# Kernel optimization log

Measured on AMD Instinct MI355X. Metric: run time of the kernel, lower is better.

## Reference

```python
import jax, jax.numpy as jnp
import numpy as np

N, F, S, D = 8, 16, 196, 1024
H = 8
HD = D // H
L = 1 + F * S  # global feature token + f*s patch tokens


def _ln(x, g, b, eps=1e-5):
    m = x.mean(-1, keepdims=True)
    v = ((x - m) ** 2).mean(-1, keepdims=True)
    return (x - m) / jnp.sqrt(v + eps) * g + b


def _attn(q, k, v, hd):
    s = jnp.einsum('bqd,bkd->bqk', q, k) / jnp.sqrt(jnp.asarray(hd, q.dtype))
    return jnp.einsum('bqk,bkd->bqd', jax.nn.softmax(s, axis=-1), v)


def setup_inputs() -> dict:
    key = jax.random.key(0)
    ks = jax.random.split(key, 8)
    sc = 0.02
    return {
        'x': jax.random.normal(ks[0], (N, L, D), jnp.float32),
        'W_in': jax.random.normal(ks[1], (D, D), jnp.float32) * sc,
        'b_in': jnp.zeros((D,), jnp.float32),
        'g_in': jnp.ones((D,), jnp.float32),
        'beta_in': jnp.zeros((D,), jnp.float32),
        'W_q': jax.random.normal(ks[2], (D, D), jnp.float32) * sc,
        'W_k': jax.random.normal(ks[3], (D, D), jnp.float32) * sc,
        'W_v': jax.random.normal(ks[4], (D, D), jnp.float32) * sc,
        'g_out': jnp.ones((D,), jnp.float32),
        'beta_out': jnp.zeros((D,), jnp.float32),
        'W_out': jax.random.normal(ks[5], (D, D), jnp.float32) * sc,
        'b_out': jnp.zeros((D,), jnp.float32),
        'att_type': 1,  # 1 == 'time', 0 == 'space' (static)
    }


def reference(x, W_in, b_in, g_in, beta_in, W_q, W_k, W_v, g_out, beta_out, W_out, b_out, att_type):
    n = x.shape[0]
    nh = n * H
    # in_fc: Linear + LayerNorm
    x = _ln(x @ W_in + b_in, g_in, beta_in)
    q, k, v = x @ W_q, x @ W_k, x @ W_v

    def split_heads(y):  # [n, L, D] -> [n*h, L, hd]
        return y.reshape(n, L, H, HD).transpose(0, 2, 1, 3).reshape(nh, L, HD)

    q, k, v = map(split_heads, (q, k, v))
    feat_q, q = q[:, :1], q[:, 1:]
    feat_k, k = k[:, :1], k[:, 1:]
    feat_v, v = v[:, :1], v[:, 1:]

    # token_att is computed in the original but never used (dead code):
    # token_att = _attn(feat_q, k, v, HD)

    if att_type == 1:  # time attention: windows of length F per spatial site
        qt = q.reshape(nh, F, S, HD).transpose(0, 2, 1, 3).reshape(nh * S, F, HD)
        kt = k.reshape(nh, F, S, HD).transpose(0, 2, 1, 3).reshape(nh * S, F, HD)
        vt = v.reshape(nh, F, S, HD).transpose(0, 2, 1, 3).reshape(nh * S, F, HD)
        fk = jnp.tile(feat_k, (S, 1, 1))  # torch .repeat(s,1,1)
        fv = jnp.tile(feat_v, (S, 1, 1))
        kk = jnp.concatenate((fk, kt), axis=1)  # [nh*s, 1+f, hd]
        vv = jnp.concatenate((fv, vt), axis=1)
        seq = _attn(qt, kk, vv, HD)  # [nh*s, f, hd]
        seq = seq.reshape(nh, S, F, HD).transpose(0, 2, 1, 3).reshape(nh, F * S, HD)
    else:  # space attention: windows of length S per frame
        qs = q.reshape(nh * F, S, HD)
        ks_ = k.reshape(nh * F, S, HD)
        vs = v.reshape(nh * F, S, HD)
        fk = jnp.tile(feat_k, (F, 1, 1))
        fv = jnp.tile(feat_v, (F, 1, 1))
        kk = jnp.concatenate((fk, ks_), axis=1)  # [nh*f, 1+s, hd]
        vv = jnp.concatenate((fv, vs), axis=1)
        seq = _attn(qs, kk, vv, HD)  # [nh*f, s, hd]
        seq = seq.reshape(nh, F * S, HD)

    out = jnp.concatenate((feat_q, seq), axis=1)  # [nh, L, hd]
    out = out.reshape(n, H, L, HD).transpose(0, 2, 1, 3).reshape(n, L, D)
    out = _ln(out, g_out, beta_out) @ W_out + b_out
    return out
```

## Files before the change

kernel.cpp:

```cpp
#include <hip/hip_runtime.h>
#include <stdint.h>

#define N_B 8
#define F_T 16
#define S_T 196
#define D_M 1024
#define H_N 8
#define HD  128
#define L_T 3137
#define M_R (N_B * L_T)
#define M_P 25216

typedef __attribute__((ext_vector_type(8))) short bf16x8;
typedef __attribute__((ext_vector_type(4))) float f32x4;

__device__ __forceinline__ float b2f(unsigned int u) {
  union { unsigned int i; float f; } x; x.i = u << 16; return x.f;
}
__device__ __forceinline__ unsigned short f2b(float f) {
  union { float f; unsigned int i; } x; x.f = f;
  unsigned int r = x.i + 0x7fffu + ((x.i >> 16) & 1u);
  return (unsigned short)(r >> 16);
}

__global__ __launch_bounds__(256) void convert_pad(const float* __restrict__ x,
                                                   unsigned short* __restrict__ xb,
                                                   int nreal) {
  int i = (blockIdx.x * 256 + threadIdx.x) * 4;
  float4 v;
  if (i < nreal) v = *(const float4*)(x + i);
  else { v.x = 0.f; v.y = 0.f; v.z = 0.f; v.w = 0.f; }
  ushort4 o;
  o.x = f2b(v.x); o.y = f2b(v.y); o.z = f2b(v.z); o.w = f2b(v.w);
  *(ushort4*)(xb + i) = o;
}

struct WP { const float* s[5]; unsigned short* d[5]; };
__global__ __launch_bounds__(256) void transpose5(WP p) {
  __shared__ float t[32][33];
  const int w = blockIdx.z;
  const float* W = p.s[w];
  unsigned short* Wt = p.d[w];
  const int tx = threadIdx.x, ty = threadIdx.y;
  const int n0 = blockIdx.x * 32, k0 = blockIdx.y * 32;
#pragma unroll
  for (int i = 0; i < 4; i++)
    t[ty + i * 8][tx] = W[(size_t)(k0 + ty + i * 8) * D_M + n0 + tx];
  __syncthreads();
#pragma unroll
  for (int i = 0; i < 4; i++)
    Wt[(size_t)(n0 + ty + i * 8) * D_M + k0 + tx] = f2b(t[tx][ty + i * 8]);
}

__device__ __forceinline__ void async16(const unsigned short* g, unsigned short* l) {
  __builtin_amdgcn_global_load_lds((const __attribute__((address_space(1))) void*)g,
                                   (__attribute__((address_space(3))) void*)l, 16, 0, 0);
}

struct Outs { void* p[3]; };

#define MFMA_Q(AV, MLO)                                                        \
  __builtin_amdgcn_s_setprio(1);                                               \
  _Pragma("unroll") for (int m_ = 0; m_ < 4; ++m_)                             \
      _Pragma("unroll") for (int n_ = 0; n_ < 4; ++n_)                         \
          acc[(MLO) + m_][n_] = __builtin_amdgcn_mfma_f32_16x16x32_bf16(       \
              AV[(MLO) + m_], bv[n_], acc[(MLO) + m_][n_], 0, 0, 0);           \
  __builtin_amdgcn_s_setprio(0);

#define TILE_ONE(T, BUF, STGB, STGA, VMN)                                      \
  do {                                                                         \
    const unsigned short* Ab = sA + (BUF) * 16384 + aOff;                      \
    const unsigned short* Bb = sB + (BUF) * 16384 + bOff;                      \
    if (STGB) {                                                                \
      async16(gB + ((T) + 1) * 64,          sBst + (1 - (BUF)) * 16384);       \
      async16(gB + ((T) + 1) * 64 + 65536,  sBst + (1 - (BUF)) * 16384 + 4096);\
    }                                                                          \
    _Pragma("unroll") for (int m_ = 0; m_ < 4; ++m_)                           \
        av0[m_] = *(const bf16x8*)(Ab + m_ * 1024 + sl0);                      \
    _Pragma("unroll") for (int n_ = 0; n_ < 4; ++n_)                           \
        bv[n_] = *(const bf16x8*)(Bb + n_ * 1024 + sl0);                       \
    _Pragma("unroll") for (int m_ = 0; m_ < 4; ++m_)                           \
        av1[m_] = *(const bf16x8*)(Ab + m_ * 1024 + sl1);                      \
    MFMA_Q(av0, 0)                                                             \
    if (STGB) {                                                                \
      async16(gB + ((T) + 1) * 64 + 131072, sBst + (1 - (BUF)) * 16384 + 8192);\
      async16(gB + ((T) + 1) * 64 + 196608, sBst + (1 - (BUF)) * 16384 + 12288);\
    }                                                                          \
    _Pragma("unroll") for (int m_ = 0; m_ < 4; ++m_)                           \
        av0[4 + m_] = *(const bf16x8*)(Ab + (4 + m_) * 1024 + sl0);            \
    _Pragma("unroll") for (int m_ = 0; m_ < 4; ++m_)                           \
        av1[4 + m_] = *(const bf16x8*)(Ab + (4 + m_) * 1024 + sl1);            \
    MFMA_Q(av0, 4)                                                             \
    asm volatile("s_waitcnt lgkmcnt(0)" ::: "memory");                         \
    __builtin_amdgcn_s_barrier();                                              \
    asm volatile("" ::: "memory");                                             \
    if (STGA) {                                                                \
      async16(gA + ((T) + 2) * 64,          sAst + (BUF) * 16384);             \
      async16(gA + ((T) + 2) * 64 + 65536,  sAst + (BUF) * 16384 + 4096);      \
    }                                                                          \
    _Pragma("unroll") for (int n_ = 0; n_ < 4; ++n_)                           \
        bv[n_] = *(const bf16x8*)(Bb + n_ * 1024 + sl1);                       \
    MFMA_Q(av1, 0)                                                             \
    if (STGA) {                                                                \
      async16(gA + ((T) + 2) * 64 + 131072, sAst + (BUF) * 16384 + 8192);      \
      async16(gA + ((T) + 2) * 64 + 196608, sAst + (BUF) * 16384 + 12288);     \
    }                                                                          \
    MFMA_Q(av1, 4)                                                             \
    if ((VMN) == 4)                                                            \
      asm volatile("s_waitcnt vmcnt(4) lgkmcnt(0)" ::: "memory");              \
    else if ((VMN) == 0)                                                       \
      asm volatile("s_waitcnt vmcnt(0) lgkmcnt(0)" ::: "memory");              \
    else                                                                       \
      asm volatile("s_waitcnt lgkmcnt(0)" ::: "memory");                       \
    __builtin_amdgcn_s_barrier();                                              \
    asm volatile("" ::: "memory");                                             \
  } while (0)

template <int MODE>
__global__ __launch_bounds__(512, 2) void gemm_bt(const unsigned short* __restrict__ A,
                                                  const unsigned short* __restrict__ Bt,
                                                  const float* __restrict__ bias,
                                                  Outs o, int Mreal) {
  __shared__ __align__(16) unsigned short lds[65536];
  unsigned short* sA = lds;
  unsigned short* sB = lds + 32768;

  const int tid = threadIdx.x;
  const int lane = tid & 63;
  const int wv = tid >> 6;
  const int wm = wv >> 2, wn = wv & 3;
  const int l15 = lane & 15, kg = lane >> 4;

  constexpr int NCT = (MODE == 3) ? 12 : 4;
  constexpr int NWG = 99 * NCT;
  constexpr int Q8 = NWG >> 3, R8 = NWG & 7;
  const int xcd = blockIdx.x & 7, off = blockIdx.x >> 3;
  const int lin = (xcd < R8 ? xcd * (Q8 + 1) : R8 * (Q8 + 1) + (xcd - R8) * Q8) + off;
  const int band = lin / 396;
  const int rem = lin - band * 396;
  const int rowBase = (rem >> 2) * 256;
  const int colBase = (band * 4 + (rem & 3)) * 256;

  const int srow = lane >> 3;
  const int gk = ((lane & 7) ^ srow) * 8;
  const unsigned short* gA = A + (size_t)(rowBase + wv * 8 + srow) * 1024 + gk;
  const unsigned short* gB = Bt + (size_t)(colBase + wv * 8 + srow) * 1024 + gk;
  unsigned short* sAst = sA + wv * 512 + lane * 8;
  unsigned short* sBst = sB + wv * 512 + lane * 8;

  const int aOff = (wm * 128 + l15) * 64;
  const int bOff = (wn * 64 + l15) * 64;
  const int sl0 = ((kg) ^ (l15 & 7)) * 8;
  const int sl1 = ((4 + kg) ^ (l15 & 7)) * 8;

  f32x4 acc[8][4] = {};
  bf16x8 av0[8], av1[8], bv[4];

#pragma unroll
  for (int i = 0; i < 4; i++) async16(gA + i * 65536, sAst + i * 4096);
#pragma unroll
  for (int i = 0; i < 4; i++) async16(gB + i * 65536, sBst + i * 4096);
#pragma unroll
  for (int i = 0; i < 4; i++) async16(gA + i * 65536 + 64, sAst + 16384 + i * 4096);
  asm volatile("s_waitcnt vmcnt(4)" ::: "memory");
  __builtin_amdgcn_s_barrier();
  asm volatile("" ::: "memory");

#pragma unroll 1
  for (int tp = 0; tp < 7; ++tp) {
    const int t0 = tp * 2;
    TILE_ONE(t0, 0, true, true, 4);
    TILE_ONE(t0 + 1, 1, true, true, 4);
  }
  TILE_ONE(14, 0, true, false, 0);
  TILE_ONE(15, 1, false, false, -1);

  __syncthreads();
  if (MODE == 2) {
    float* Cf = (float*)lds;
    float* outF = (float*)o.p[0];
#pragma unroll
    for (int p = 0; p < 2; ++p) {
      if (p) __syncthreads();
      if (wm == p) {
#pragma unroll
        for (int n = 0; n < 4; ++n) {
          const int col = wn * 64 + n * 16 + l15;
          const float bval = bias[colBase + col];
#pragma unroll
          for (int m = 0; m < 8; ++m)
#pragma unroll
            for (int r = 0; r < 4; ++r)
              Cf[(m * 16 + kg * 4 + r) * 256 + col] = acc[m][n][r] + bval;
        }
      }
      __syncthreads();
#pragma unroll
      for (int t2 = 0; t2 < 16; ++t2) {
        const int g = t2 * 512 + tid;
        const int row = g >> 6, ch = g & 63;
        const int grow = rowBase + p * 128 + row;
        if (grow < Mreal)
          *(float4*)(outF + (size_t)grow * 1024 + colBase + ch * 4) =
              *(const float4*)(Cf + row * 256 + ch * 4);
      }
    }
  } else {
    unsigned short* Cs = lds;
#pragma unroll
    for (int n = 0; n < 4; ++n) {
      const int col = wn * 64 + n * 16 + l15;
      const float bval = (MODE == 1) ? bias[colBase + col] : 0.f;
#pragma unroll
      for (int m = 0; m < 8; ++m)
#pragma unroll
        for (int r = 0; r < 4; ++r)
          Cs[(wm * 128 + m * 16 + kg * 4 + r) * 256 + col] = f2b(acc[m][n][r] + bval);
    }
    __syncthreads();
    unsigned short* C;
    int cbase;
    if (MODE == 3) { C = (unsigned short*)o.p[colBase >> 10]; cbase = colBase & 1023; }
    else { C = (unsigned short*)o.p[0]; cbase = colBase; }
#pragma unroll
    for (int t2 = 0; t2 < 16; ++t2) {
      const int g = t2 * 512 + tid;
      const int row = g >> 5, ch = g & 31;
      const int grow = rowBase + row;
      if (grow < Mreal)
        *(uint4*)(C + (size_t)grow * 1024 + cbase + ch * 8) =
            *(const uint4*)(Cs + row * 256 + ch * 8);
    }
  }
}

__global__ __launch_bounds__(256) void ln_kernel(const unsigned short* __restrict__ src,
                                                 const unsigned short* __restrict__ src0,
                                                 const float* __restrict__ g,
                                                 const float* __restrict__ beta,
                                                 unsigned short* __restrict__ out, int Mreal) {
  const int row = blockIdx.x, tid = threadIdx.x;
  unsigned short* op = out + (size_t)row * 1024 + tid * 4;
  if (row >= Mreal) {
    ushort4 z; z.x = 0; z.y = 0; z.z = 0; z.w = 0;
    *(ushort4*)op = z;
    return;
  }
  const unsigned short* s = src;
  if (src0 != nullptr && (row % L_T) == 0) s = src0;
  const unsigned short* ip = s + (size_t)row * 1024 + tid * 4;
  uint2 raw = *(const uint2*)ip;
  float x0 = b2f(raw.x & 0xffffu), x1 = b2f(raw.x >> 16);
  float x2 = b2f(raw.y & 0xffffu), x3 = b2f(raw.y >> 16);
  float sum = x0 + x1 + x2 + x3;
  float sq = x0 * x0 + x1 * x1 + x2 * x2 + x3 * x3;
#pragma unroll
  for (int off = 32; off > 0; off >>= 1) {
    sum += __shfl_down(sum, off);
    sq += __shfl_down(sq, off);
  }
  __shared__ float red[8];
  if ((tid & 63) == 0) { red[tid >> 6] = sum; red[4 + (tid >> 6)] = sq; }
  __syncthreads();
  const float ts = red[0] + red[1] + red[2] + red[3];
  const float tq = red[4] + red[5] + red[6] + red[7];
  const float mean = ts * (1.f / 1024.f);
  const float var = tq * (1.f / 1024.f) - mean * mean;
  const float rstd = rsqrtf(var + 1e-5f);
  const float4 gv = *(const float4*)(g + tid * 4);
  const float4 bv = *(const float4*)(beta + tid * 4);
  ushort4 o;
  o.x = f2b((x0 - mean) * rstd * gv.x + bv.x);
  o.y = f2b((x1 - mean) * rstd * gv.y + bv.y);
  o.z = f2b((x2 - mean) * rstd * gv.z + bv.z);
  o.w = f2b((x3 - mean) * rstd * gv.w + bv.w);
  *(ushort4*)op = o;
}

#define ATT_T_BLOCKS (64 * 49)
__global__ __launch_bounds__(256) void attn_kernel(const unsigned short* __restrict__ q,
                                                   const unsigned short* __restrict__ k,
                                                   const unsigned short* __restrict__ v,
                                                   unsigned short* __restrict__ out,
                                                   const int* __restrict__ att_type) {
  __shared__ __align__(16) char smem[22528];
  const int tid = threadIdx.x;
  const int bid = blockIdx.x;
  const int at = att_type[0];

  if (at == 1) {
    if (bid >= ATT_T_BLOCKS) return;
    const int lane = tid & 63, wv = tid >> 6;
    const int l15 = lane & 15, kg = lane >> 4;
    const int hb = bid / 49, sb = bid - hb * 49;
    const int s = sb * 4 + wv;
    const int n = hb >> 3, h = hb & 7;
    const int fi = (hb * S_T + s) & 63;
    const size_t frow = (size_t)(fi >> 3) * L_T;
    const int fcol = (fi & 7) * HD;
    const int qbase = n * L_T + 1 + s;
    const int hcol = h * HD;

    unsigned short* Pl = (unsigned short*)(smem + wv * 5632);
    unsigned short* Vl = (unsigned short*)(smem + wv * 5632 + 1024);

    {
      const int dim0 = l15 * 8;
#pragma unroll
      for (int p = 0; p < 5; p++) {
        const int key = p * 4 + kg;
        if (key < 17) {
          const unsigned short* vp = (key == 0)
              ? (v + frow * 1024 + fcol + dim0)
              : (v + (size_t)(qbase + (key - 1) * S_T) * 1024 + hcol + dim0);
          uint4 r = *(const uint4*)vp;
          unsigned int* wp = (unsigned int*)Vl + key * 65 + l15 * 4;
          wp[0] = r.x; wp[1] = r.y; wp[2] = r.z; wp[3] = r.w;
        }
      }
    }

    bf16x8 aq[4], bk0[4], bk1[4];
    {
      const unsigned short* qp = q + (size_t)(qbase + l15 * S_T) * 1024 + hcol + kg * 8;
      const unsigned short* kp = (l15 == 0)
          ? (k + frow * 1024 + fcol + kg * 8)
          : (k + (size_t)(qbase + (l15 - 1) * S_T) * 1024 + hcol + kg * 8);
      const unsigned short* kp1 = k + (size_t)(qbase + 15 * S_T) * 1024 + hcol + kg * 8;
#pragma unroll
      for (int t = 0; t < 4; t++) {
        aq[t] = *(const bf16x8*)(qp + t * 32);
        bk0[t] = *(const bf16x8*)(kp + t * 32);
        if (l15 == 0) bk1[t] = *(const bf16x8*)(kp1 + t * 32);
        else {
          bf16x8 z = {};
          bk1[t] = z;
        }
      }
    }

    f32x4 c0 = {}, c1 = {};
#pragma unroll
    for (int t = 0; t < 4; t++) {
      c0 = __builtin_amdgcn_mfma_f32_16x16x32_bf16(aq[t], bk0[t], c0, 0, 0, 0);
      c1 = __builtin_amdgcn_mfma_f32_16x16x32_bf16(aq[t], bk1[t], c1, 0, 0, 0);
    }

    const float scl = 0.08838834764831845f;
#pragma unroll
    for (int r = 0; r < 4; r++) {
      float v0 = c0[r] * scl;
      float k16 = __shfl(c1[r] * scl, lane & 48);
      float mx = v0;
#pragma unroll
      for (int m = 1; m < 16; m <<= 1) mx = fmaxf(mx, __shfl_xor(mx, m));
      mx = fmaxf(mx, k16);
      float p = __expf(v0 - mx);
      float p16 = __expf(k16 - mx);
      float sum = p;
#pragma unroll
      for (int m = 1; m < 16; m <<= 1) sum += __shfl_xor(sum, m);
      sum += p16;
      const float inv = 1.f / sum;
      const int row = kg * 4 + r;
      Pl[row * 32 + l15] = f2b(p * inv);
      Pl[row * 32 + 16 + l15] = (l15 == 0) ? f2b(p16 * inv) : (unsigned short)0;
    }

    bf16x8 ap = *(const bf16x8*)(Pl + l15 * 32 + kg * 8);
#pragma unroll
    for (int nt = 0; nt < 8; nt++) {
      const int dim = nt * 16 + l15;
      bf16x8 bvv;
#pragma unroll
      for (int j = 0; j < 8; j++) {
        const int key = kg * 8 + j;
        const int kc = (key < 17) ? key : 0;
        unsigned short raw = Vl[kc * 130 + dim];
        bvv[j] = (key < 17) ? (short)raw : (short)0;
      }
      f32x4 z = {};
      f32x4 o = __builtin_amdgcn_mfma_f32_16x16x32_bf16(ap, bvv, z, 0, 0, 0);
#pragma unroll
      for (int r = 0; r < 4; r++) {
        const int qi = kg * 4 + r;
        out[(size_t)(qbase + qi * S_T) * 1024 + hcol + nt * 16 + l15] = f2b(o[r]);
      }
    }
    return;
  }

  float (*qs)[132] = (float (*)[132])smem;
  float (*sc)[212] = (float (*)[212])(smem + 8448);
  const int hb = bid / 208;
  const int rem = bid - hb * 208;
  const int f = rem / 13, qc = rem - f * 13;
  const int n = hb >> 3, h = hb & 7;
  const int fi = (hb * F_T + f) & 63;
  const size_t frow = (size_t)(fi >> 3) * L_T;
  const int fcol = (fi & 7) * HD;
  const int kbase = n * L_T + 1 + f * S_T;
  const int qbase = kbase + qc * 16;
  const int nk = S_T + 1;
  const int nqv = (qc == 12) ? 4 : 16;
  const int hcol = h * HD;

  {
    const int i = tid >> 4, db = (tid & 15) * 8;
    float* dst = &qs[i][db];
    if (i < nqv) {
      const unsigned short* qp = q + (size_t)(qbase + i) * 1024 + hcol + db;
      uint4 r = *(const uint4*)qp;
      dst[0] = b2f(r.x & 0xffffu); dst[1] = b2f(r.x >> 16);
      dst[2] = b2f(r.y & 0xffffu); dst[3] = b2f(r.y >> 16);
      dst[4] = b2f(r.z & 0xffffu); dst[5] = b2f(r.z >> 16);
      dst[6] = b2f(r.w & 0xffffu); dst[7] = b2f(r.w >> 16);
    } else {
#pragma unroll
      for (int u = 0; u < 8; u++) dst[u] = 0.f;
    }
  }
  __syncthreads();

  const int nslot = 16 * nk;
  for (int slot = tid; slot < nslot; slot += 256) {
    const int i = slot / nk, j = slot - i * nk;
    const unsigned short* kp = (j == 0)
        ? (k + frow * 1024 + fcol)
        : (k + (size_t)(kbase + (j - 1)) * 1024 + hcol);
    float acc = 0.f;
#pragma unroll 4
    for (int d = 0; d < 128; d += 8) {
      uint4 r = *(const uint4*)(kp + d);
      acc += qs[i][d + 0] * b2f(r.x & 0xffffu);
      acc += qs[i][d + 1] * b2f(r.x >> 16);
      acc += qs[i][d + 2] * b2f(r.y & 0xffffu);
      acc += qs[i][d + 3] * b2f(r.y >> 16);
      acc += qs[i][d + 4] * b2f(r.z & 0xffffu);
      acc += qs[i][d + 5] * b2f(r.z >> 16);
      acc += qs[i][d + 6] * b2f(r.w & 0xffffu);
      acc += qs[i][d + 7] * b2f(r.w >> 16);
    }
    sc[i][j] = acc * 0.08838834764831845f;
  }
  __syncthreads();

  if (tid < 16) {
    const int i = tid;
    float m = -1e30f;
    for (int j = 0; j < nk; j++) m = fmaxf(m, sc[i][j]);
    float ssum = 0.f;
    for (int j = 0; j < nk; j++) {
      float e = __expf(sc[i][j] - m);
      sc[i][j] = e;
      ssum += e;
    }
    const float inv = 1.f / ssum;
    for (int j = 0; j < nk; j++) sc[i][j] *= inv;
  }
  __syncthreads();

  {
    const int i = tid >> 4, db = (tid & 15) * 8;
    float o[8];
#pragma unroll
    for (int u = 0; u < 8; u++) o[u] = 0.f;
    for (int j = 0; j < nk; j++) {
      const unsigned short* vp = (j == 0)
          ? (v + frow * 1024 + fcol + db)
          : (v + (size_t)(kbase + (j - 1)) * 1024 + hcol + db);
      const float p = sc[i][j];
      uint4 r = *(const uint4*)vp;
      o[0] += p * b2f(r.x & 0xffffu); o[1] += p * b2f(r.x >> 16);
      o[2] += p * b2f(r.y & 0xffffu); o[3] += p * b2f(r.y >> 16);
      o[4] += p * b2f(r.z & 0xffffu); o[5] += p * b2f(r.z >> 16);
      o[6] += p * b2f(r.w & 0xffffu); o[7] += p * b2f(r.w >> 16);
    }
    if (i < nqv) {
      unsigned short* op = out + (size_t)(qbase + i) * 1024 + hcol + db;
      uint4 w;
      w.x = (unsigned)f2b(o[0]) | ((unsigned)f2b(o[1]) << 16);
      w.y = (unsigned)f2b(o[2]) | ((unsigned)f2b(o[3]) << 16);
      w.z = (unsigned)f2b(o[4]) | ((unsigned)f2b(o[5]) << 16);
      w.w = (unsigned)f2b(o[6]) | ((unsigned)f2b(o[7]) << 16);
      *(uint4*)op = w;
    }
  }
}

extern "C" void kernel_launch(void* const* d_in, const int* in_sizes, int n_in,
                              void* d_out, int out_size, void* d_ws, size_t ws_size,
                              hipStream_t stream) {
  const float* x        = (const float*)d_in[0];
  const float* W_in     = (const float*)d_in[1];
  const float* b_in     = (const float*)d_in[2];
  const float* g_in     = (const float*)d_in[3];
  const float* beta_in  = (const float*)d_in[4];
  const float* W_q      = (const float*)d_in[5];
  const float* W_k      = (const float*)d_in[6];
  const float* W_v      = (const float*)d_in[7];
  const float* g_out    = (const float*)d_in[8];
  const float* beta_out = (const float*)d_in[9];
  const float* W_out    = (const float*)d_in[10];
  const float* b_out    = (const float*)d_in[11];
  const int* att_type   = (const int*)d_in[12];
  float* out = (float*)d_out;

  char* ws = (char*)d_ws;
  const size_t MB = (size_t)M_P * 1024 * 2;
  unsigned short* xb = (unsigned short*)(ws + 0 * MB);
  unsigned short* t1 = (unsigned short*)(ws + 1 * MB);
  unsigned short* xh = (unsigned short*)(ws + 2 * MB);
  unsigned short* kb = (unsigned short*)(ws + 3 * MB);
  unsigned short* vb = (unsigned short*)(ws + 4 * MB);
  unsigned short* wt = (unsigned short*)(ws + 5 * MB);
  const size_t WSZ = (size_t)1024 * 1024;
  unsigned short* wt_in  = wt;
  unsigned short* wqkv   = wt + 1 * WSZ;
  unsigned short* wt_out = wt + 4 * WSZ;

  convert_pad<<<M_P, 256, 0, stream>>>(x, xb, M_R * 1024);

  WP wp;
  wp.s[0] = W_in; wp.s[1] = W_q; wp.s[2] = W_k; wp.s[3] = W_v; wp.s[4] = W_out;
  wp.d[0] = wt_in;
  wp.d[1] = wqkv;
  wp.d[2] = wqkv + 1 * WSZ;
  wp.d[3] = wqkv + 2 * WSZ;
  wp.d[4] = wt_out;
  transpose5<<<dim3(32, 32, 5), dim3(32, 8), 0, stream>>>(wp);

  Outs o1; o1.p[0] = t1; o1.p[1] = nullptr; o1.p[2] = nullptr;
  gemm_bt<1><<<396, 512, 0, stream>>>(xb, wt_in, b_in, o1, M_P);
  ln_kernel<<<M_P, 256, 0, stream>>>(t1, nullptr, g_in, beta_in, xh, M_R);

  Outs oq; oq.p[0] = t1; oq.p[1] = kb; oq.p[2] = vb;
  gemm_bt<3><<<1188, 512, 0, stream>>>(xh, wqkv, nullptr, oq, M_P);

  attn_kernel<<<13312, 256, 0, stream>>>(t1, kb, vb, xb, att_type);
  ln_kernel<<<M_P, 256, 0, stream>>>(xb, t1, g_out, beta_out, xh, M_R);

  Outs oo; oo.p[0] = out; oo.p[1] = nullptr; oo.p[2] = nullptr;
  gemm_bt<2><<<396, 512, 0, stream>>>(xh, wt_out, b_out, oo, M_R);
}
```

Before: 539.1 us.

## Interleave LDS reads with MFMA phases via extra barriers and swizzle epilogue staging

Restructures the GEMM inner tile into four phases separated by workgroup barriers and partial lgkmcnt waits, so waves take turns between LDS fragment loads and MFMA bursts (ping-pong style). It also trims the A-fragment register arrays from 8 to 4 entries using a third buffer, which lowers register pressure. Separately, the epilogue staging of the C tile in LDS now uses an XOR swizzle to reduce bank conflicts on both the write and read-back. The extra barriers add synchronisation cost per tile, and the partial waits rely on exact instruction counts being correct.

After: 567.3 us. 5.2% more time.

```diff
diff --git a/kernel.cpp b/kernel.cpp
--- a/kernel.cpp
+++ b/kernel.cpp
@@ -59,18 +59,19 @@
 
 struct Outs { void* p[3]; };
 
-#define MFMA_Q(AV, MLO)                                                        \
+#define MFMA16(AV, MLO)                                                        \
   __builtin_amdgcn_s_setprio(1);                                               \
   _Pragma("unroll") for (int m_ = 0; m_ < 4; ++m_)                             \
       _Pragma("unroll") for (int n_ = 0; n_ < 4; ++n_)                         \
           acc[(MLO) + m_][n_] = __builtin_amdgcn_mfma_f32_16x16x32_bf16(       \
-              AV[(MLO) + m_], bv[n_], acc[(MLO) + m_][n_], 0, 0, 0);           \
+              AV[m_], bv[n_], acc[(MLO) + m_][n_], 0, 0, 0);                   \
   __builtin_amdgcn_s_setprio(0);
 
-#define TILE_ONE(T, BUF, STGB, STGA, VMN)                                      \
+#define TILE_P(T, BUF, STGB, STGA, VMN)                                        \
   do {                                                                         \
     const unsigned short* Ab = sA + (BUF) * 16384 + aOff;                      \
     const unsigned short* Bb = sB + (BUF) * 16384 + bOff;                      \
+              \
     if (STGB) {                                                                \
       async16(gB + ((T) + 1) * 64,          sBst + (1 - (BUF)) * 16384);       \
       async16(gB + ((T) + 1) * 64 + 65536,  sBst + (1 - (BUF)) * 16384 + 4096);\
@@ -81,37 +82,45 @@
         bv[n_] = *(const bf16x8*)(Bb + n_ * 1024 + sl0);                       \
     _Pragma("unroll") for (int m_ = 0; m_ < 4; ++m_)                           \
         av1[m_] = *(const bf16x8*)(Ab + m_ * 1024 + sl1);                      \
-    MFMA_Q(av0, 0)                                                             \
+    __builtin_amdgcn_s_barrier();                                              \
+    asm volatile("s_waitcnt lgkmcnt(4)" ::: "memory");                         \
+    MFMA16(av0, 0)                                                             \
+    __builtin_amdgcn_s_barrier();                                              \
+                    \
     if (STGB) {                                                                \
       async16(gB + ((T) + 1) * 64 + 131072, sBst + (1 - (BUF)) * 16384 + 8192);\
       async16(gB + ((T) + 1) * 64 + 196608, sBst + (1 - (BUF)) * 16384 + 12288);\
     }                                                                          \
     _Pragma("unroll") for (int m_ = 0; m_ < 4; ++m_)                           \
-        av0[4 + m_] = *(const bf16x8*)(Ab + (4 + m_) * 1024 + sl0);            \
+        av0[m_] = *(const bf16x8*)(Ab + (4 + m_) * 1024 + sl0);                \
     _Pragma("unroll") for (int m_ = 0; m_ < 4; ++m_)                           \
-        av1[4 + m_] = *(const bf16x8*)(Ab + (4 + m_) * 1024 + sl1);            \
-    MFMA_Q(av0, 4)                                                             \
+        av2[m_] = *(const bf16x8*)(Ab + (4 + m_) * 1024 + sl1);                \
+    __builtin_amdgcn_s_barrier();                                              \
     asm volatile("s_waitcnt lgkmcnt(0)" ::: "memory");                         \
-    __builtin_amdgcn_s_barrier();                                              \
-    asm volatile("" ::: "memory");                                             \
+    MFMA16(av0, 4)                                                             \
+    __builtin_amdgcn_s_barrier();                                              \
+                        \
     if (STGA) {                                                                \
       async16(gA + ((T) + 2) * 64,          sAst + (BUF) * 16384);             \
       async16(gA + ((T) + 2) * 64 + 65536,  sAst + (BUF) * 16384 + 4096);      \
     }                                                                          \
     _Pragma("unroll") for (int n_ = 0; n_ < 4; ++n_)                           \
         bv[n_] = *(const bf16x8*)(Bb + n_ * 1024 + sl1);                       \
-    MFMA_Q(av1, 0)                                                             \
+    __builtin_amdgcn_s_barrier();                                              \
+    asm volatile("s_waitcnt lgkmcnt(0)" ::: "memory");                         \
+    MFMA16(av1, 0)                                                             \
+    __builtin_amdgcn_s_barrier();                                              \
+                    \
     if (STGA) {                                                                \
       async16(gA + ((T) + 2) * 64 + 131072, sAst + (BUF) * 16384 + 8192);      \
       async16(gA + ((T) + 2) * 64 + 196608, sAst + (BUF) * 16384 + 12288);     \
     }                                                                          \
-    MFMA_Q(av1, 4)                                                             \
+    __builtin_amdgcn_s_barrier();                                              \
+    MFMA16(av2, 4)                                                             \
     if ((VMN) == 4)                                                            \
-      asm volatile("s_waitcnt vmcnt(4) lgkmcnt(0)" ::: "memory");              \
+      asm volatile("s_waitcnt vmcnt(4)" ::: "memory");                         \
     else if ((VMN) == 0)                                                       \
-      asm volatile("s_waitcnt vmcnt(0) lgkmcnt(0)" ::: "memory");              \
-    else                                                                       \
-      asm volatile("s_waitcnt lgkmcnt(0)" ::: "memory");                       \
+      asm volatile("s_waitcnt vmcnt(0)" ::: "memory");                         \
     __builtin_amdgcn_s_barrier();                                              \
     asm volatile("" ::: "memory");                                             \
   } while (0)
@@ -154,7 +163,7 @@
   const int sl1 = ((4 + kg) ^ (l15 & 7)) * 8;
 
   f32x4 acc[8][4] = {};
-  bf16x8 av0[8], av1[8], bv[4];
+  bf16x8 av0[4], av1[4], av2[4], bv[4];
 
 #pragma unroll
   for (int i = 0; i < 4; i++) async16(gA + i * 65536, sAst + i * 4096);
@@ -169,11 +178,11 @@
 #pragma unroll 1
   for (int tp = 0; tp < 7; ++tp) {
     const int t0 = tp * 2;
-    TILE_ONE(t0, 0, true, true, 4);
-    TILE_ONE(t0 + 1, 1, true, true, 4);
-  }
-  TILE_ONE(14, 0, true, false, 0);
-  TILE_ONE(15, 1, false, false, -1);
+    TILE_P(t0, 0, true, true, 4);
+    TILE_P(t0 + 1, 1, true, true, 4);
+  }
+  TILE_P(14, 0, true, false, 0);
+  TILE_P(15, 1, false, false, -1);
 
   __syncthreads();
   if (MODE == 2) {
@@ -187,11 +196,15 @@
         for (int n = 0; n < 4; ++n) {
           const int col = wn * 64 + n * 16 + l15;
           const float bval = bias[colBase + col];
+          const int gc = col >> 2, c3 = col & 3;
 #pragma unroll
           for (int m = 0; m < 8; ++m)
 #pragma unroll
-            for (int r = 0; r < 4; ++r)
-              Cf[(m * 16 + kg * 4 + r) * 256 + col] = acc[m][n][r] + bval;
+            for (int r = 0; r < 4; ++r) {
+              const int row = m * 16 + kg * 4 + r;
+              const int gs = gc ^ (((row >> 2) & 7) << 2);
+              Cf[row * 256 + gs * 4 + c3] = acc[m][n][r] + bval;
+            }
         }
       }
       __syncthreads();
@@ -199,10 +212,11 @@
       for (int t2 = 0; t2 < 16; ++t2) {
         const int g = t2 * 512 + tid;
         const int row = g >> 6, ch = g & 63;
+        const int slot = ch ^ (((row >> 2) & 7) << 2);
         const int grow = rowBase + p * 128 + row;
         if (grow < Mreal)
           *(float4*)(outF + (size_t)grow * 1024 + colBase + ch * 4) =
-              *(const float4*)(Cf + row * 256 + ch * 4);
+              *(const float4*)(Cf + row * 256 + slot * 4);
       }
     }
   } else {
@@ -211,11 +225,15 @@
     for (int n = 0; n < 4; ++n) {
       const int col = wn * 64 + n * 16 + l15;
       const float bval = (MODE == 1) ? bias[colBase + col] : 0.f;
+      const int gc = col >> 3, c7 = col & 7;
 #pragma unroll
       for (int m = 0; m < 8; ++m)
 #pragma unroll
-        for (int r = 0; r < 4; ++r)
-          Cs[(wm * 128 + m * 16 + kg * 4 + r) * 256 + col] = f2b(acc[m][n][r] + bval);
+        for (int r = 0; r < 4; ++r) {
+          const int row = wm * 128 + m * 16 + kg * 4 + r;
+          const int gs = gc ^ ((row & 7) << 2);
+          Cs[row * 256 + gs * 8 + c7] = f2b(acc[m][n][r] + bval);
+        }
     }
     __syncthreads();
     unsigned short* C;
@@ -226,10 +244,11 @@
     for (int t2 = 0; t2 < 16; ++t2) {
       const int g = t2 * 512 + tid;
       const int row = g >> 5, ch = g & 31;
+      const int slot = ch ^ ((row & 7) << 2);
       const int grow = rowBase + row;
       if (grow < Mreal)
         *(uint4*)(C + (size_t)grow * 1024 + cbase + ch * 8) =
-            *(const uint4*)(Cs + row * 256 + ch * 8);
+            *(const uint4*)(Cs + row * 256 + slot * 8);
     }
   }
 }
```
